# Kernel optimization log

Hardware: AMD Instinct MI355X
Metric: run time of the kernel (lower is better)

The kernel has to match this reference:

```python
import jax, jax.numpy as jnp
import numpy as np
import math

IN_F = 256
OUT_F = 256
HEADS = 4
HEAD_DIM = OUT_F // HEADS
B, N = 4, 2048


def setup_inputs() -> dict:
    key = jax.random.key(0)
    ks = jax.random.split(key, 7)
    s = 1.0 / math.sqrt(IN_F)
    h = jax.random.normal(ks[0], (B, N, IN_F), dtype=jnp.float32)
    adj = jax.random.randint(ks[1], (N, N), 0, 2, dtype=jnp.int32)
    Wq = jax.random.uniform(ks[2], (IN_F, OUT_F), jnp.float32, -s, s)
    Wk = jax.random.uniform(ks[3], (IN_F, OUT_F), jnp.float32, -s, s)
    Wv = jax.random.uniform(ks[4], (IN_F, OUT_F), jnp.float32, -s, s)
    Wo = jax.random.uniform(ks[5], (OUT_F, OUT_F), jnp.float32, -s, s)
    bo = jax.random.uniform(ks[6], (OUT_F,), jnp.float32, -s, s)
    return {"h": h, "adj": adj, "Wq": Wq, "Wk": Wk, "Wv": Wv, "Wo": Wo, "bo": bo}


def reference(h, adj, Wq, Wk, Wv, Wo, bo):
    Bv, Nv, _ = h.shape
    # project and split heads: [B, H, N, Dh]
    q = (h @ Wq).reshape(Bv, Nv, HEADS, HEAD_DIM).transpose(0, 2, 1, 3)
    k = (h @ Wk).reshape(Bv, Nv, HEADS, HEAD_DIM).transpose(0, 2, 1, 3)
    v = (h @ Wv).reshape(Bv, Nv, HEADS, HEAD_DIM).transpose(0, 2, 1, 3)
    scores = jnp.einsum('bhnd,bhmd->bhnm', q, k) / math.sqrt(HEAD_DIM)
    mask = (adj == 0)[None, None, :, :]  # [1,1,N,N]
    scores = jnp.where(mask, jnp.float32(-1e9), scores)
    attn = jax.nn.softmax(scores, axis=-1)  # dropout is identity in eval / p=0
    out = jnp.einsum('bhnm,bhmd->bhnd', attn, v)
    out = out.transpose(0, 2, 1, 3).reshape(Bv, Nv, OUT_F)
    return h + out @ Wo + bo
```

## Files before the change

### kernel.cpp

```cpp
#include <hip/hip_runtime.h>
#include <hip/hip_bf16.h>

#define B_ 4
#define N_ 2048
#define F_ 256
#define H_ 4
#define D_ 64

typedef __attribute__((ext_vector_type(8))) short short8;
typedef __attribute__((ext_vector_type(4))) float f32x4;
typedef __attribute__((ext_vector_type(4))) unsigned u32x4;

__device__ __forceinline__ unsigned short f2bf(float x) {
  unsigned u = __builtin_bit_cast(unsigned, x);
  u = (u + 0x7fffu + ((u >> 16) & 1u)) >> 16;
  return (unsigned short)u;
}

__device__ __forceinline__ float bf2f(unsigned short x) {
  unsigned u = ((unsigned)x) << 16;
  return __builtin_bit_cast(float, u);
}

__device__ __forceinline__ f32x4 mfma16(short8 a, short8 b, f32x4 c) {
  return __builtin_amdgcn_mfma_f32_16x16x32_bf16(a, b, c, 0, 0, 0);
}

#define QSCALE 0.1803368801111204f

__global__ __launch_bounds__(256) void prep_kernel(
    const float* __restrict__ h, const int* __restrict__ adj,
    const float* __restrict__ Wq, const float* __restrict__ Wk,
    const float* __restrict__ Wv, const float* __restrict__ Wo,
    unsigned short* __restrict__ hbf,
    unsigned short* __restrict__ wqt, unsigned short* __restrict__ wkt,
    unsigned short* __restrict__ wvt, unsigned short* __restrict__ wot,
    unsigned* __restrict__ adjt) {
  int bid = blockIdx.x;
  int tid = threadIdx.x;
  if (bid < 2048) {
    int idx = (bid * 256 + tid) * 4;
    float4 v = *(const float4*)(h + idx);
    ushort4 o;
    o.x = f2bf(v.x); o.y = f2bf(v.y); o.z = f2bf(v.z); o.w = f2bf(v.w);
    *(ushort4*)(hbf + idx) = o;
  } else if (bid < 3072) {
    int t = (bid - 2048) * 256 + tid;
    int w = t >> 16;
    int e = t & 65535;
    int i = e >> 8;
    int o = e & 255;
    const float* W = (w == 0) ? Wq : (w == 1) ? Wk : (w == 2) ? Wv : Wo;
    unsigned short* Wt = (w == 0) ? wqt : (w == 1) ? wkt : (w == 2) ? wvt : wot;
    Wt[o * 256 + i] = f2bf(W[i * 256 + o]);
  } else {
    int lane = tid & 63;
    int wid = (bid - 3072) * 4 + (tid >> 6);
    #pragma unroll
    for (int it = 0; it < 16; ++it) {
      int widx = wid * 16 + it;
      int n = widx >> 5;
      int mw64 = widx & 31;
      unsigned long long m = __ballot(adj[widx * 64 + lane] != 0);
      if (lane == 0) {
        adjt[(2 * mw64) * 2048 + n] = (unsigned)m;
        adjt[(2 * mw64 + 1) * 2048 + n] = (unsigned)(m >> 32);
      }
    }
  }
}

__global__ __launch_bounds__(256) void qkv_gemm(
    const unsigned short* __restrict__ hbf,
    const unsigned short* __restrict__ wqt, const unsigned short* __restrict__ wkt,
    const unsigned short* __restrict__ wvt,
    unsigned short* __restrict__ qb, unsigned short* __restrict__ kb,
    unsigned short* __restrict__ vtb) {
  int lane = threadIdx.x & 63;
  int wv = threadIdx.x >> 6;
  int g = lane >> 4;
  int c = lane & 15;
  int row32 = blockIdx.x * 128 + wv * 32;
  int colbase = blockIdx.y * 64;
  int which = colbase >> 8;
  int fbase = colbase & 255;
  const unsigned short* wt = (which == 0) ? wqt : (which == 1) ? wkt : wvt;

  f32x4 acc[2][4];
  #pragma unroll
  for (int rt = 0; rt < 2; ++rt)
    #pragma unroll
    for (int cc = 0; cc < 4; ++cc) acc[rt][cc] = (f32x4){0.f, 0.f, 0.f, 0.f};

  for (int k = 0; k < 256; k += 32) {
    short8 a[2], b[4];
    #pragma unroll
    for (int rt = 0; rt < 2; ++rt)
      a[rt] = *(const short8*)(hbf + (row32 + rt * 16 + c) * 256 + k + g * 8);
    #pragma unroll
    for (int cc = 0; cc < 4; ++cc)
      b[cc] = *(const short8*)(wt + (fbase + cc * 16 + c) * 256 + k + g * 8);
    #pragma unroll
    for (int rt = 0; rt < 2; ++rt)
      #pragma unroll
      for (int cc = 0; cc < 4; ++cc)
        acc[rt][cc] = mfma16(a[rt], b[cc], acc[rt][cc]);
  }

  #pragma unroll
  for (int rt = 0; rt < 2; ++rt) {
    #pragma unroll
    for (int cc = 0; cc < 4; ++cc) {
      #pragma unroll
      for (int r = 0; r < 4; ++r) {
        int row = row32 + rt * 16 + g * 4 + r;
        int f = fbase + cc * 16 + c;
        int hh = f >> 6, d = f & 63;
        int bb = row >> 11, n = row & 2047;
        float v = acc[rt][cc][r];
        if (which == 0)
          qb[((bb * H_ + hh) * N_ + n) * D_ + d] = f2bf(v * QSCALE);
        else if (which == 1)
          kb[((bb * H_ + hh) * N_ + n) * D_ + d] = f2bf(v);
        else
          vtb[((bb * H_ + hh) * D_ + d) * N_ + n] = f2bf(v);
      }
    }
  }
}

__global__ __launch_bounds__(256) void attn_kernel(
    const unsigned short* __restrict__ qb, const unsigned short* __restrict__ kb,
    const unsigned short* __restrict__ vtb, const unsigned* __restrict__ adjt,
    unsigned short* __restrict__ Opart, float* __restrict__ Lp) {
  __shared__ __align__(16) unsigned short plds[4][2][32 * 40];
  int lane = threadIdx.x & 63;
  int wv = threadIdx.x >> 6;
  int g = lane >> 4;
  int c = lane & 15;
  int lb = (blockIdx.x & 7) * 128 + (blockIdx.x >> 3);
  int bh = lb >> 6;
  int qt = lb & 63;
  int s = wv;
  int task = bh * 256 + qt * 4 + s;
  int qbase = qt * 32;
  const unsigned short* Qp = qb + bh * (N_ * D_);
  const unsigned short* Kp = kb + bh * (N_ * D_);
  const unsigned short* Vt = vtb + bh * (D_ * N_);

  short8 qf[2][2];
  #pragma unroll
  for (int rt = 0; rt < 2; ++rt)
    #pragma unroll
    for (int dh = 0; dh < 2; ++dh)
      qf[rt][dh] = *(const short8*)(Qp + (qbase + rt * 16 + c) * D_ + dh * 32 + g * 8);

  f32x4 O[2][4];
  float Lsum[2][4];
  #pragma unroll
  for (int rt = 0; rt < 2; ++rt) {
    #pragma unroll
    for (int dt = 0; dt < 4; ++dt) O[rt][dt] = (f32x4){0.f, 0.f, 0.f, 0.f};
    #pragma unroll
    for (int r = 0; r < 4; ++r) Lsum[rt][r] = 0.f;
  }

  const f32x4 z4 = {0.f, 0.f, 0.f, 0.f};
  int kv0 = s * 512;

  short8 kfa[2][2], kfb[2][2];
  #pragma unroll
  for (int mt = 0; mt < 2; ++mt)
    #pragma unroll
    for (int dh = 0; dh < 2; ++dh)
      kfa[mt][dh] = *(const short8*)(Kp + (kv0 + mt * 16 + c) * D_ + dh * 32 + g * 8);

  for (int it = 0; it < 16; ++it) {
    int mb = kv0 + it * 32;
    int mw = mb >> 5;
    int nmb = (it == 15) ? kv0 : (mb + 32);
    #pragma unroll
    for (int mt = 0; mt < 2; ++mt)
      #pragma unroll
      for (int dh = 0; dh < 2; ++dh)
        kfb[mt][dh] = *(const short8*)(Kp + (nmb + mt * 16 + c) * D_ + dh * 32 + g * 8);
    u32x4 awq[2];
    #pragma unroll
    for (int rt = 0; rt < 2; ++rt)
      awq[rt] = *(const u32x4*)(adjt + mw * 2048 + qbase + rt * 16 + g * 4);

    f32x4 S[2][2];
    #pragma unroll
    for (int rt = 0; rt < 2; ++rt)
      #pragma unroll
      for (int mt = 0; mt < 2; ++mt) {
        f32x4 ss = mfma16(qf[rt][0], kfa[mt][0], z4);
        S[rt][mt] = mfma16(qf[rt][1], kfa[mt][1], ss);
      }

    unsigned short* myp = plds[wv][it & 1];
    #pragma unroll
    for (int rt = 0; rt < 2; ++rt) {
      #pragma unroll
      for (int r = 0; r < 4; ++r) {
        unsigned aw = awq[rt][r];
        float e0 = __builtin_amdgcn_exp2f(S[rt][0][r]);
        float e1 = __builtin_amdgcn_exp2f(S[rt][1][r]);
        float p0 = ((aw >> c) & 1u) ? e0 : 0.f;
        float p1 = ((aw >> (c + 16)) & 1u) ? e1 : 0.f;
        Lsum[rt][r] += p0 + p1;
        unsigned pr;
        asm("v_cvt_pk_bf16_f32 %0, %1, %2" : "=v"(pr) : "v"(p0), "v"(p1));
        int prow = rt * 16 + g * 4 + r;
        myp[prow * 40 + c] = (unsigned short)pr;
        myp[prow * 40 + 16 + c] = (unsigned short)(pr >> 16);
      }
    }

    short8 pa[2];
    #pragma unroll
    for (int rt = 0; rt < 2; ++rt)
      pa[rt] = *(const short8*)(myp + (rt * 16 + c) * 40 + g * 8);

    #pragma unroll
    for (int dt = 0; dt < 4; ++dt) {
      short8 vf = *(const short8*)(Vt + (dt * 16 + c) * N_ + mb + g * 8);
      #pragma unroll
      for (int rt = 0; rt < 2; ++rt)
        O[rt][dt] = mfma16(pa[rt], vf, O[rt][dt]);
    }

    #pragma unroll
    for (int mt = 0; mt < 2; ++mt)
      #pragma unroll
      for (int dh = 0; dh < 2; ++dh)
        kfa[mt][dh] = kfb[mt][dh];
  }

  unsigned short* Ob = Opart + (size_t)task * 2048;
  #pragma unroll
  for (int rt = 0; rt < 2; ++rt) {
    #pragma unroll
    for (int r = 0; r < 4; ++r) {
      float l = Lsum[rt][r];
      l += __shfl_xor(l, 1);
      l += __shfl_xor(l, 2);
      l += __shfl_xor(l, 4);
      l += __shfl_xor(l, 8);
      int row = rt * 16 + g * 4 + r;
      if (c == 0) Lp[task * 32 + row] = l;
      #pragma unroll
      for (int dt = 0; dt < 4; ++dt)
        Ob[row * 64 + dt * 16 + c] = f2bf(O[rt][dt][r]);
    }
  }
}

__global__ __launch_bounds__(256) void combine_kernel(
    const unsigned short* __restrict__ Opart, const float* __restrict__ Lp,
    unsigned short* __restrict__ ao) {
  int t = blockIdx.x * 256 + threadIdx.x;
  int dq = t & 3;
  int n = (t >> 2) & 2047;
  int bh = t >> 13;
  int qt = n >> 5, row32 = n & 31;
  int tbase = bh * 256 + qt * 4;

  float Lg = 0.f;
  #pragma unroll
  for (int s = 0; s < 4; ++s) Lg += Lp[(tbase + s) * 32 + row32];
  float inv = 1.0f / Lg;

  float o[16];
  #pragma unroll
  for (int d = 0; d < 16; ++d) o[d] = 0.f;
  #pragma unroll
  for (int s = 0; s < 4; ++s) {
    const unsigned short* p = Opart + (size_t)(tbase + s) * 2048 + row32 * 64 + dq * 16;
    short8 v0 = *(const short8*)(p);
    short8 v1 = *(const short8*)(p + 8);
    #pragma unroll
    for (int d = 0; d < 8; ++d) {
      o[d]     += bf2f((unsigned short)v0[d]);
      o[8 + d] += bf2f((unsigned short)v1[d]);
    }
  }

  int bb = bh >> 2, hh = bh & 3;
  short8 ob0, ob1;
  #pragma unroll
  for (int d = 0; d < 8; ++d) {
    ob0[d] = (short)f2bf(o[d] * inv);
    ob1[d] = (short)f2bf(o[8 + d] * inv);
  }
  unsigned short* dst = ao + ((size_t)(bb * N_ + n)) * F_ + hh * 64 + dq * 16;
  *(short8*)(dst) = ob0;
  *(short8*)(dst + 8) = ob1;
}

__global__ __launch_bounds__(256) void out_gemm(
    const unsigned short* __restrict__ ao, const unsigned short* __restrict__ wot,
    const float* __restrict__ h, const float* __restrict__ bo,
    float* __restrict__ out) {
  int lane = threadIdx.x & 63;
  int wv = threadIdx.x >> 6;
  int g = lane >> 4;
  int c = lane & 15;
  int row16 = blockIdx.x * 64 + wv * 16;
  int colb = blockIdx.y * 64;
  int arow = row16 + c;

  f32x4 acc[4];
  #pragma unroll
  for (int cc = 0; cc < 4; ++cc) acc[cc] = (f32x4){0.f, 0.f, 0.f, 0.f};

  for (int k = 0; k < 256; k += 32) {
    short8 a = *(const short8*)(ao + arow * 256 + k + g * 8);
    #pragma unroll
    for (int cc = 0; cc < 4; ++cc) {
      short8 bfrag = *(const short8*)(wot + (colb + cc * 16 + c) * 256 + k + g * 8);
      acc[cc] = mfma16(a, bfrag, acc[cc]);
    }
  }

  #pragma unroll
  for (int cc = 0; cc < 4; ++cc) {
    #pragma unroll
    for (int r = 0; r < 4; ++r) {
      int row = row16 + g * 4 + r;
      int col = colb + cc * 16 + c;
      out[row * 256 + col] = h[row * 256 + col] + bo[col] + acc[cc][r];
    }
  }
}

extern "C" void kernel_launch(void* const* d_in, const int* in_sizes, int n_in,
                              void* d_out, int out_size, void* d_ws, size_t ws_size,
                              hipStream_t stream) {
  (void)in_sizes; (void)n_in; (void)out_size; (void)ws_size;
  const float* h  = (const float*)d_in[0];
  const int* adj  = (const int*)d_in[1];
  const float* Wq = (const float*)d_in[2];
  const float* Wk = (const float*)d_in[3];
  const float* Wv = (const float*)d_in[4];
  const float* Wo = (const float*)d_in[5];
  const float* bo = (const float*)d_in[6];
  float* out = (float*)d_out;

  char* ws = (char*)d_ws;
  unsigned short* hbf = (unsigned short*)(ws + 0);
  unsigned short* wqt = (unsigned short*)(ws + 4194304);
  unsigned short* wkt = (unsigned short*)(ws + 4325376);
  unsigned short* wvt = (unsigned short*)(ws + 4456448);
  unsigned short* wot = (unsigned short*)(ws + 4587520);
  unsigned*       adjt = (unsigned*)(ws + 4718592);
  unsigned short* qb  = (unsigned short*)(ws + 5242880);
  unsigned short* kb  = (unsigned short*)(ws + 9437184);
  unsigned short* vtb = (unsigned short*)(ws + 13631488);
  unsigned short* ao  = (unsigned short*)(ws + 17825792);
  unsigned short* Opart = (unsigned short*)(ws + 22020096);
  float*          Lp  = (float*)(ws + 38797312);

  prep_kernel<<<4096, 256, 0, stream>>>(h, adj, Wq, Wk, Wv, Wo,
                                        hbf, wqt, wkt, wvt, wot, adjt);
  qkv_gemm<<<dim3(64, 12), 256, 0, stream>>>(hbf, wqt, wkt, wvt, qb, kb, vtb);
  attn_kernel<<<1024, 256, 0, stream>>>(qb, kb, vtb, adjt, Opart, Lp);
  combine_kernel<<<512, 256, 0, stream>>>(Opart, Lp, ao);
  out_gemm<<<dim3(128, 4), 256, 0, stream>>>(ao, wot, h, bo, out);
}
```

Measured before the change: 199.9 us.

## Stage weight tiles in LDS, prefetch V fragments, add setprio and occupancy hints

The QKV and output GEMMs now copy their 64-column weight tile into padded shared memory once per block, so waves stop re-reading it from global memory. The attention kernel double-buffers V fragments in registers alongside K, so the next tile's loads overlap the current tile's math. It also unrolls the KV loop by two, raises wave priority around MFMA sections, and adds a min-blocks launch bound. In exchange, register pressure rises and the occupancy hint may force spills, and the GEMMs use extra LDS plus a sync.

```diff
diff --git a/kernel.cpp b/kernel.cpp
--- a/kernel.cpp
+++ b/kernel.cpp
@@ -76,6 +76,7 @@
     const unsigned short* __restrict__ wvt,
     unsigned short* __restrict__ qb, unsigned short* __restrict__ kb,
     unsigned short* __restrict__ vtb) {
+  __shared__ __align__(16) unsigned short blds[64 * 264];
   int lane = threadIdx.x & 63;
   int wv = threadIdx.x >> 6;
   int g = lane >> 4;
@@ -86,6 +87,13 @@
   int fbase = colbase & 255;
   const unsigned short* wt = (which == 0) ? wqt : (which == 1) ? wkt : wvt;
 
+  for (int i = threadIdx.x; i < 64 * 32; i += 256) {
+    int col = i >> 5;
+    int kc = (i & 31) * 8;
+    *(short8*)(blds + col * 264 + kc) = *(const short8*)(wt + (fbase + col) * 256 + kc);
+  }
+  __syncthreads();
+
   f32x4 acc[2][4];
   #pragma unroll
   for (int rt = 0; rt < 2; ++rt)
@@ -99,7 +107,7 @@
       a[rt] = *(const short8*)(hbf + (row32 + rt * 16 + c) * 256 + k + g * 8);
     #pragma unroll
     for (int cc = 0; cc < 4; ++cc)
-      b[cc] = *(const short8*)(wt + (fbase + cc * 16 + c) * 256 + k + g * 8);
+      b[cc] = *(const short8*)(blds + (cc * 16 + c) * 264 + k + g * 8);
     #pragma unroll
     for (int rt = 0; rt < 2; ++rt)
       #pragma unroll
@@ -129,7 +137,7 @@
   }
 }
 
-__global__ __launch_bounds__(256) void attn_kernel(
+__global__ __launch_bounds__(256, 4) void attn_kernel(
     const unsigned short* __restrict__ qb, const unsigned short* __restrict__ kb,
     const unsigned short* __restrict__ vtb, const unsigned* __restrict__ adjt,
     unsigned short* __restrict__ Opart, float* __restrict__ Lp) {
@@ -168,13 +176,17 @@
   const f32x4 z4 = {0.f, 0.f, 0.f, 0.f};
   int kv0 = s * 512;
 
-  short8 kfa[2][2], kfb[2][2];
+  short8 kfa[2][2], kfb[2][2], vfa[4], vfb[4];
   #pragma unroll
   for (int mt = 0; mt < 2; ++mt)
     #pragma unroll
     for (int dh = 0; dh < 2; ++dh)
       kfa[mt][dh] = *(const short8*)(Kp + (kv0 + mt * 16 + c) * D_ + dh * 32 + g * 8);
-
+  #pragma unroll
+  for (int dt = 0; dt < 4; ++dt)
+    vfa[dt] = *(const short8*)(Vt + (dt * 16 + c) * N_ + kv0 + g * 8);
+
+  #pragma unroll 2
   for (int it = 0; it < 16; ++it) {
     int mb = kv0 + it * 32;
     int mw = mb >> 5;
@@ -184,11 +196,15 @@
       #pragma unroll
       for (int dh = 0; dh < 2; ++dh)
         kfb[mt][dh] = *(const short8*)(Kp + (nmb + mt * 16 + c) * D_ + dh * 32 + g * 8);
+    #pragma unroll
+    for (int dt = 0; dt < 4; ++dt)
+      vfb[dt] = *(const short8*)(Vt + (dt * 16 + c) * N_ + nmb + g * 8);
     u32x4 awq[2];
     #pragma unroll
     for (int rt = 0; rt < 2; ++rt)
       awq[rt] = *(const u32x4*)(adjt + mw * 2048 + qbase + rt * 16 + g * 4);
 
+    __builtin_amdgcn_s_setprio(1);
     f32x4 S[2][2];
     #pragma unroll
     for (int rt = 0; rt < 2; ++rt)
@@ -197,6 +213,7 @@
         f32x4 ss = mfma16(qf[rt][0], kfa[mt][0], z4);
         S[rt][mt] = mfma16(qf[rt][1], kfa[mt][1], ss);
       }
+    __builtin_amdgcn_s_setprio(0);
 
     unsigned short* myp = plds[wv][it & 1];
     #pragma unroll
@@ -222,19 +239,23 @@
     for (int rt = 0; rt < 2; ++rt)
       pa[rt] = *(const short8*)(myp + (rt * 16 + c) * 40 + g * 8);
 
+    __builtin_amdgcn_s_setprio(1);
     #pragma unroll
     for (int dt = 0; dt < 4; ++dt) {
-      short8 vf = *(const short8*)(Vt + (dt * 16 + c) * N_ + mb + g * 8);
       #pragma unroll
       for (int rt = 0; rt < 2; ++rt)
-        O[rt][dt] = mfma16(pa[rt], vf, O[rt][dt]);
-    }
+        O[rt][dt] = mfma16(pa[rt], vfa[dt], O[rt][dt]);
+    }
+    __builtin_amdgcn_s_setprio(0);
 
     #pragma unroll
     for (int mt = 0; mt < 2; ++mt)
       #pragma unroll
       for (int dh = 0; dh < 2; ++dh)
         kfa[mt][dh] = kfb[mt][dh];
+    #pragma unroll
+    for (int dt = 0; dt < 4; ++dt)
+      vfa[dt] = vfb[dt];
   }
 
   unsigned short* Ob = Opart + (size_t)task * 2048;
@@ -302,6 +323,7 @@
     const unsigned short* __restrict__ ao, const unsigned short* __restrict__ wot,
     const float* __restrict__ h, const float* __restrict__ bo,
     float* __restrict__ out) {
+  __shared__ __align__(16) unsigned short blds[64 * 264];
   int lane = threadIdx.x & 63;
   int wv = threadIdx.x >> 6;
   int g = lane >> 4;
@@ -310,6 +332,13 @@
   int colb = blockIdx.y * 64;
   int arow = row16 + c;
 
+  for (int i = threadIdx.x; i < 64 * 32; i += 256) {
+    int col = i >> 5;
+    int kc = (i & 31) * 8;
+    *(short8*)(blds + col * 264 + kc) = *(const short8*)(wot + (colb + col) * 256 + kc);
+  }
+  __syncthreads();
+
   f32x4 acc[4];
   #pragma unroll
   for (int cc = 0; cc < 4; ++cc) acc[cc] = (f32x4){0.f, 0.f, 0.f, 0.f};
@@ -318,7 +347,7 @@
     short8 a = *(const short8*)(ao + arow * 256 + k + g * 8);
     #pragma unroll
     for (int cc = 0; cc < 4; ++cc) {
-      short8 bfrag = *(const short8*)(wot + (colb + cc * 16 + c) * 256 + k + g * 8);
+      short8 bfrag = *(const short8*)(blds + (cc * 16 + c) * 264 + k + g * 8);
       acc[cc] = mfma16(a, bfrag, acc[cc]);
     }
   }
```

Result: slower. 330.6 us (+65.4%).
